# Kernel tuning notes

Measured on AMD Instinct MI355X. Metric: run time of the kernel, lower is better.

Reference implementation:

```python
import jax, jax.numpy as jnp
import numpy as np

N_NODES = 100000


def gcn_layer(x, W, b, src, dst, norm, n):
    # x: [N, Fin] -> linear transform then normalized scatter-add aggregation
    h = x @ W                                   # [N, Fout]
    msgs = h[src] * norm[:, None]               # [E+N, Fout] edge messages
    out = jax.ops.segment_sum(msgs, dst, num_segments=n)
    return out + b


def _build_graph(edge_index, n):
    # add self loops (PyG GCNConv default)
    loops = jnp.arange(n, dtype=edge_index.dtype)
    src = jnp.concatenate([edge_index[0], loops])
    dst = jnp.concatenate([edge_index[1], loops])
    deg = jax.ops.segment_sum(jnp.ones_like(dst, dtype=jnp.float32), dst, num_segments=n)
    dis = jnp.where(deg > 0, jax.lax.rsqrt(deg), 0.0)  # deg^{-1/2}
    norm = dis[src] * dis[dst]                  # symmetric normalization per edge
    return src, dst, norm


def setup_inputs() -> dict:
    key = jax.random.key(0)
    ks = jax.random.split(key, 8)
    x = jax.random.normal(ks[0], (N_NODES, 3), dtype=jnp.float32)
    edge_index = jax.random.randint(ks[1], (2, 6400000), 0, N_NODES, dtype=jnp.int32)
    def glorot(k, fin, fout):
        s = jnp.sqrt(6.0 / (fin + fout))
        return jax.random.uniform(k, (fin, fout), jnp.float32, -s, s)
    return {
        "x": x,
        "edge_index": edge_index,
        "W1": glorot(ks[2], 3, 32), "b1": jnp.zeros((32,), jnp.float32),
        "W2": glorot(ks[3], 32, 32), "b2": jnp.zeros((32,), jnp.float32),
        "W3": glorot(ks[4], 32, 1), "b3": jnp.zeros((1,), jnp.float32),
    }


def reference(x, edge_index, W1, b1, W2, b2, W3, b3):
    n = x.shape[0]
    src, dst, norm = _build_graph(edge_index, n)
    h = jax.nn.relu(gcn_layer(x, W1, b1, src, dst, norm, n))
    h = jax.nn.relu(gcn_layer(h, W2, b2, src, dst, norm, n))
    return gcn_layer(h, W3, b3, src, dst, norm, n)
```

## Files before the change

### kernel.cpp

```cpp
#include <hip/hip_runtime.h>
#include <hip/hip_fp16.h>


#define BLK 256
#define SB 1280
#define CHUNK 5000
#define BKT 128
#define NBKT 782
#define MAXNB 1024
#define BUFSZ 15360

__global__ void k_hist(const int* __restrict__ dst, int* __restrict__ hist, int E) {
    __shared__ int lh[NBKT];
    for (int b = threadIdx.x; b < NBKT; b += blockDim.x) lh[b] = 0;
    __syncthreads();
    int beg = blockIdx.x * CHUNK;
    int end = min(E, beg + CHUNK);
    int nq = (end - beg) >> 2;
    const int4* d4 = (const int4*)(dst + beg);
    for (int i = threadIdx.x; i < nq; i += blockDim.x) {
        int4 d = d4[i];
        atomicAdd(&lh[d.x >> 7], 1);
        atomicAdd(&lh[d.y >> 7], 1);
        atomicAdd(&lh[d.z >> 7], 1);
        atomicAdd(&lh[d.w >> 7], 1);
    }
    for (int e = beg + (nq << 2) + threadIdx.x; e < end; e += blockDim.x)
        atomicAdd(&lh[dst[e] >> 7], 1);
    __syncthreads();
    for (int b = threadIdx.x; b < NBKT; b += blockDim.x)
        hist[(size_t)blockIdx.x * NBKT + b] = lh[b];
}

__global__ void k_scanA(const int* __restrict__ hist, int* __restrict__ histX,
                        int* __restrict__ btot, int NB) {
    int b = blockIdx.x, t = threadIdx.x;
    int base = t * 5;
    int v0 = hist[(size_t)(base + 0) * NB + b];
    int v1 = hist[(size_t)(base + 1) * NB + b];
    int v2 = hist[(size_t)(base + 2) * NB + b];
    int v3 = hist[(size_t)(base + 3) * NB + b];
    int v4 = hist[(size_t)(base + 4) * NB + b];
    int s = v0 + v1 + v2 + v3 + v4;
    int lane = t & 63, w = t >> 6;
    int x = s;
#pragma unroll
    for (int off = 1; off < 64; off <<= 1) {
        int u = __shfl_up(x, off, 64);
        if (lane >= off) x += u;
    }
    __shared__ int wsum[4];
    if (lane == 63) wsum[w] = x;
    __syncthreads();
    int woff = 0;
    for (int k = 0; k < 4; k++) woff += (k < w) ? wsum[k] : 0;
    int run = woff + x - s;
    histX[(size_t)(base + 0) * NB + b] = run;  run += v0;
    histX[(size_t)(base + 1) * NB + b] = run;  run += v1;
    histX[(size_t)(base + 2) * NB + b] = run;  run += v2;
    histX[(size_t)(base + 3) * NB + b] = run;  run += v3;
    histX[(size_t)(base + 4) * NB + b] = run;  run += v4;
    if (t == 255) btot[b] = run;
}

__global__ void k_scanB(const int* __restrict__ btot, int* __restrict__ bbase,
                        int NB, int E) {
    __shared__ int sh[MAXNB];
    int t = threadIdx.x;
    int v = (t < NB) ? btot[t] : 0;
    sh[t] = v;
    __syncthreads();
    for (int off = 1; off < MAXNB; off <<= 1) {
        int u = (t >= off) ? sh[t - off] : 0;
        __syncthreads();
        sh[t] += u;
        __syncthreads();
    }
    if (t < NB) bbase[t] = sh[t] - v;
    if (t == 0) bbase[NB] = E;
}

__global__ void k_bsort(const int* __restrict__ src, const int* __restrict__ dst,
                        const int* __restrict__ hist, const int* __restrict__ histX,
                        const int* __restrict__ bbase,
                        unsigned int* __restrict__ packed, int E) {
    __shared__ unsigned int bufB[CHUNK];
    __shared__ unsigned short binarr2[CHUNK];
    __shared__ int cnt[NBKT];
    __shared__ int off[NBKT];
    __shared__ int cur[NBKT];
    __shared__ int gbase[NBKT];
    __shared__ int wsum[4];
    int t = threadIdx.x;
    int beg = blockIdx.x * CHUNK;
    int end = min(E, beg + CHUNK);
    int len = end - beg;
    for (int b = t; b < NBKT; b += blockDim.x) {
        cnt[b] = hist[(size_t)blockIdx.x * NBKT + b];
        gbase[b] = bbase[b] + histX[(size_t)blockIdx.x * NBKT + b];
    }
    __syncthreads();
    {
        int base = t * 4;
        int v0 = (base + 0 < NBKT) ? cnt[base + 0] : 0;
        int v1 = (base + 1 < NBKT) ? cnt[base + 1] : 0;
        int v2 = (base + 2 < NBKT) ? cnt[base + 2] : 0;
        int v3 = (base + 3 < NBKT) ? cnt[base + 3] : 0;
        int s = v0 + v1 + v2 + v3;
        int lane = t & 63, w = t >> 6;
        int x = s;
#pragma unroll
        for (int o = 1; o < 64; o <<= 1) {
            int u = __shfl_up(x, o, 64);
            if (lane >= o) x += u;
        }
        if (lane == 63) wsum[w] = x;
        __syncthreads();
        int woff = 0;
        for (int k = 0; k < 4; k++) woff += (k < w) ? wsum[k] : 0;
        int run = woff + x - s;
        if (base + 0 < NBKT) { off[base + 0] = run; cur[base + 0] = run; } run += v0;
        if (base + 1 < NBKT) { off[base + 1] = run; cur[base + 1] = run; } run += v1;
        if (base + 2 < NBKT) { off[base + 2] = run; cur[base + 2] = run; } run += v2;
        if (base + 3 < NBKT) { off[base + 3] = run; cur[base + 3] = run; } run += v3;
    }
    __syncthreads();
    for (int i = t; i < len; i += blockDim.x) {
        int d = dst[beg + i];
        int s = src[beg + i];
        int b = d >> 7;
        int pos = atomicAdd(&cur[b], 1);
        bufB[pos] = (unsigned)s | ((unsigned)(d & 127) << 17);
        binarr2[pos] = (unsigned short)b;
    }
    __syncthreads();
    for (int i = t; i < len; i += blockDim.x) {
        int b = binarr2[i];
        packed[gbase[b] + i - off[b]] = bufB[i];
    }
}

__global__ void k_sort(unsigned int* __restrict__ packed, const int* __restrict__ bbase,
                       const float* __restrict__ x, float* __restrict__ dis,
                       float4* __restrict__ y4, int* __restrict__ rowptr, int N, int E) {
    __shared__ unsigned int buf[BUFSZ];
    __shared__ int cnt[BKT];
    __shared__ int sc[BKT];
    __shared__ int cur[BKT];
    int b = blockIdx.x, t = threadIdx.x;
    int beg = bbase[b], end = bbase[b + 1];
    int len = end - beg;
    for (int i = t; i < len; i += blockDim.x) buf[i] = packed[beg + i];
    if (t < BKT) cnt[t] = 0;
    __syncthreads();
    for (int i = t; i < len; i += blockDim.x)
        atomicAdd(&cnt[buf[i] >> 17], 1);
    __syncthreads();
    int v = 0;
    if (t < BKT) { v = cnt[t]; sc[t] = v; }
    __syncthreads();
    for (int off = 1; off < BKT; off <<= 1) {
        int u = 0;
        if (t < BKT && t >= off) u = sc[t - off];
        __syncthreads();
        if (t < BKT) sc[t] += u;
        __syncthreads();
    }
    if (t < BKT) {
        int excl = sc[t] - v;
        cur[t] = excl;
        int gi = b * BKT + t;
        if (gi < N) {
            rowptr[gi] = beg + excl;
            float di = rsqrtf((float)v + 1.0f);
            dis[gi] = di;
            float4 y;
            y.x = di * x[3 * gi + 0];
            y.y = di * x[3 * gi + 1];
            y.z = di * x[3 * gi + 2];
            y.w = 0.0f;
            y4[gi] = y;
        }
    }
    __syncthreads();
    for (int i = t; i < len; i += blockDim.x) {
        unsigned vv = buf[i];
        int pos = atomicAdd(&cur[vv >> 17], 1);
        packed[beg + pos] = vv & 0x1FFFF;
    }
    if (b == 0 && t == 0) rowptr[N] = E;
}

__global__ void k_l1(const unsigned int* __restrict__ csr, const int* __restrict__ rowptr,
                     const float4* __restrict__ y4, const float* __restrict__ dis,
                     const float* __restrict__ W1, const float* __restrict__ b1,
                     __half* __restrict__ g, int N) {
    int t = blockIdx.x * blockDim.x + threadIdx.x;
    int i = t >> 5, j = t & 31;
    if (i >= N) return;
    int beg = rowptr[i], end = rowptr[i + 1];
    float ax = 0.f, ay = 0.f, az = 0.f;
    for (int e = beg + j; e < end; e += 32) {
        float4 yv = y4[__builtin_nontemporal_load(&csr[e])];
        ax += yv.x; ay += yv.y; az += yv.z;
    }
#pragma unroll
    for (int m = 16; m >= 1; m >>= 1) {
        ax += __shfl_xor(ax, m, 32);
        ay += __shfl_xor(ay, m, 32);
        az += __shfl_xor(az, m, 32);
    }
    float di = dis[i];
    float4 ys = y4[i];
    float a0 = di * (ax + ys.x);
    float a1 = di * (ay + ys.y);
    float a2 = di * (az + ys.z);
    float h = b1[j] + a0 * W1[j] + a1 * W1[32 + j] + a2 * W1[64 + j];
    g[(size_t)i * 32 + j] = __float2half(di * fmaxf(h, 0.f));
}

__global__ void k_l2(const unsigned int* __restrict__ csr, const int* __restrict__ rowptr,
                     const __half* __restrict__ g, const float* __restrict__ dis,
                     const float* __restrict__ W2, const float* __restrict__ b2,
                     const float* __restrict__ W3, float* __restrict__ q, int N) {
    int t = blockIdx.x * blockDim.x + threadIdx.x;
    int i = t >> 5, j = t & 31;
    if (i >= N) return;
    int beg = rowptr[i], end = rowptr[i + 1];
    float a0 = 0.f, a1 = 0.f, a2 = 0.f, a3 = 0.f;
    float a4 = 0.f, a5 = 0.f, a6 = 0.f, a7 = 0.f;
    for (int k0 = beg; k0 < end; k0 += 32) {
        int e = k0 + j;
        int myedge = (e < end) ? (int)__builtin_nontemporal_load(&csr[e]) : 0;
        int cnt = min(32, end - k0);
        int t2 = 0;
        for (; t2 + 8 <= cnt; t2 += 8) {
            int s0 = __shfl(myedge, t2 + 0, 32);
            int s1 = __shfl(myedge, t2 + 1, 32);
            int s2 = __shfl(myedge, t2 + 2, 32);
            int s3 = __shfl(myedge, t2 + 3, 32);
            int s4 = __shfl(myedge, t2 + 4, 32);
            int s5 = __shfl(myedge, t2 + 5, 32);
            int s6 = __shfl(myedge, t2 + 6, 32);
            int s7 = __shfl(myedge, t2 + 7, 32);
            a0 += __half2float(g[(size_t)s0 * 32 + j]);
            a1 += __half2float(g[(size_t)s1 * 32 + j]);
            a2 += __half2float(g[(size_t)s2 * 32 + j]);
            a3 += __half2float(g[(size_t)s3 * 32 + j]);
            a4 += __half2float(g[(size_t)s4 * 32 + j]);
            a5 += __half2float(g[(size_t)s5 * 32 + j]);
            a6 += __half2float(g[(size_t)s6 * 32 + j]);
            a7 += __half2float(g[(size_t)s7 * 32 + j]);
        }
        for (; t2 < cnt; t2++) {
            int s = __shfl(myedge, t2, 32);
            a0 += __half2float(g[(size_t)s * 32 + j]);
        }
    }
    float acc = ((a0 + a1) + (a2 + a3)) + ((a4 + a5) + (a6 + a7));
    float di = dis[i];
    float a = di * (acc + __half2float(g[(size_t)i * 32 + j]));
    float o = b2[j];
#pragma unroll
    for (int k = 0; k < 32; k++)
        o += __shfl(a, k, 32) * W2[k * 32 + j];
    float h2 = fmaxf(o, 0.f);
    float c = h2 * W3[j];
#pragma unroll
    for (int m = 16; m >= 1; m >>= 1)
        c += __shfl_xor(c, m, 32);
    if (j == 0) q[i] = di * c;
}

__global__ void k_l3(const unsigned int* __restrict__ csr, const int* __restrict__ rowptr,
                     const float* __restrict__ q, const float* __restrict__ dis,
                     const float* __restrict__ b3, float* __restrict__ out, int N) {
    int t = blockIdx.x * blockDim.x + threadIdx.x;
    int i = t >> 5, j = t & 31;
    if (i >= N) return;
    int beg = rowptr[i], end = rowptr[i + 1];
    float acc = 0.f;
    for (int e = beg + j; e < end; e += 32)
        acc += q[__builtin_nontemporal_load(&csr[e])];
#pragma unroll
    for (int m = 16; m >= 1; m >>= 1)
        acc += __shfl_xor(acc, m, 32);
    if (j == 0) out[i] = dis[i] * (acc + q[i]) + b3[0];
}

extern "C" void kernel_launch(void* const* d_in, const int* in_sizes, int n_in,
                              void* d_out, int out_size, void* d_ws, size_t ws_size,
                              hipStream_t stream) {
    const float* x  = (const float*)d_in[0];
    const int*   ei = (const int*)d_in[1];
    const float* W1 = (const float*)d_in[2];
    const float* b1 = (const float*)d_in[3];
    const float* W2 = (const float*)d_in[4];
    const float* b2 = (const float*)d_in[5];
    const float* W3 = (const float*)d_in[6];
    const float* b3 = (const float*)d_in[7];
    float* out = (float*)d_out;

    int N = in_sizes[0] / 3;
    int E = in_sizes[1] / 2;
    const int* src = ei;
    const int* dst = ei + E;

    char* w = (char*)d_ws;
    int*   hist   = (int*)w;       w += (size_t)SB * NBKT * 4;
    int*   histX  = (int*)w;       w += (size_t)SB * NBKT * 4;
    int*   btot   = (int*)w;       w += (size_t)MAXNB * 4;
    int*   bbase  = (int*)w;       w += (size_t)(MAXNB + 1) * 4;
    int*   rowptr = (int*)w;       w += (size_t)(N + 1) * 4;
    float* dis    = (float*)w;     w += (size_t)N * 4;
    float* y4     = (float*)w;     w += (size_t)N * 16;
    __half* g     = (__half*)w;    w += (size_t)N * 32 * 2;
    float* q      = (float*)w;     w += (size_t)N * 4;
    unsigned int* packed = (unsigned int*)w;  w += (size_t)E * 4;

    k_hist <<<SB, BLK, 0, stream>>>(dst, hist, E);
    k_scanA<<<NBKT, BLK, 0, stream>>>(hist, histX, btot, NBKT);
    k_scanB<<<1, MAXNB, 0, stream>>>(btot, bbase, NBKT, E);
    k_bsort<<<SB, BLK, 0, stream>>>(src, dst, hist, histX, bbase, packed, E);
    k_sort <<<NBKT, BLK, 0, stream>>>(packed, bbase, x, dis, (float4*)y4, rowptr, N, E);

    long long tn32 = (long long)N * 32;
    unsigned gn32 = (unsigned)((tn32 + BLK - 1) / BLK);
    k_l1<<<gn32, BLK, 0, stream>>>(packed, rowptr, (const float4*)y4, dis, W1, b1, g, N);
    k_l2<<<gn32, BLK, 0, stream>>>(packed, rowptr, g, dis, W2, b2, W3, q, N);
    k_l3<<<gn32, BLK, 0, stream>>>(packed, rowptr, q, dis, b3, out, N);
}
```

Baseline: 379.7 us.

## Split bucket sort into count and permute kernels, fusing layer-1 aggregation

```diff
diff --git a/kernel.cpp b/kernel.cpp
--- a/kernel.cpp
+++ b/kernel.cpp
@@ -8,7 +8,7 @@
 #define BKT 128
 #define NBKT 782
 #define MAXNB 1024
-#define BUFSZ 15360
+#define CAP 44
 
 __global__ void k_hist(const int* __restrict__ dst, int* __restrict__ hist, int E) {
     __shared__ int lh[NBKT];
@@ -140,21 +140,17 @@
     }
 }
 
-__global__ void k_sort(unsigned int* __restrict__ packed, const int* __restrict__ bbase,
-                       const float* __restrict__ x, float* __restrict__ dis,
-                       float4* __restrict__ y4, int* __restrict__ rowptr, int N, int E) {
-    __shared__ unsigned int buf[BUFSZ];
+__global__ void k_cnt(const unsigned int* __restrict__ packed, const int* __restrict__ bbase,
+                      const float* __restrict__ x, float* __restrict__ dis,
+                      float4* __restrict__ y4, int* __restrict__ rowptr, int N, int E) {
     __shared__ int cnt[BKT];
     __shared__ int sc[BKT];
-    __shared__ int cur[BKT];
     int b = blockIdx.x, t = threadIdx.x;
     int beg = bbase[b], end = bbase[b + 1];
-    int len = end - beg;
-    for (int i = t; i < len; i += blockDim.x) buf[i] = packed[beg + i];
     if (t < BKT) cnt[t] = 0;
     __syncthreads();
-    for (int i = t; i < len; i += blockDim.x)
-        atomicAdd(&cnt[buf[i] >> 17], 1);
+    for (int i = beg + t; i < end; i += blockDim.x)
+        atomicAdd(&cnt[packed[i] >> 17], 1);
     __syncthreads();
     int v = 0;
     if (t < BKT) { v = cnt[t]; sc[t] = v; }
@@ -167,11 +163,9 @@
         __syncthreads();
     }
     if (t < BKT) {
-        int excl = sc[t] - v;
-        cur[t] = excl;
         int gi = b * BKT + t;
         if (gi < N) {
-            rowptr[gi] = beg + excl;
+            rowptr[gi] = beg + sc[t] - v;
             float di = rsqrtf((float)v + 1.0f);
             dis[gi] = di;
             float4 y;
@@ -182,41 +176,57 @@
             y4[gi] = y;
         }
     }
-    __syncthreads();
-    for (int i = t; i < len; i += blockDim.x) {
-        unsigned vv = buf[i];
-        int pos = atomicAdd(&cur[vv >> 17], 1);
-        packed[beg + pos] = vv & 0x1FFFF;
-    }
     if (b == 0 && t == 0) rowptr[N] = E;
 }
 
-__global__ void k_l1(const unsigned int* __restrict__ csr, const int* __restrict__ rowptr,
-                     const float4* __restrict__ y4, const float* __restrict__ dis,
-                     const float* __restrict__ W1, const float* __restrict__ b1,
-                     __half* __restrict__ g, int N) {
-    int t = blockIdx.x * blockDim.x + threadIdx.x;
-    int i = t >> 5, j = t & 31;
-    if (i >= N) return;
-    int beg = rowptr[i], end = rowptr[i + 1];
-    float ax = 0.f, ay = 0.f, az = 0.f;
-    for (int e = beg + j; e < end; e += 32) {
-        float4 yv = y4[__builtin_nontemporal_load(&csr[e])];
-        ax += yv.x; ay += yv.y; az += yv.z;
-    }
-#pragma unroll
-    for (int m = 16; m >= 1; m >>= 1) {
-        ax += __shfl_xor(ax, m, 32);
-        ay += __shfl_xor(ay, m, 32);
-        az += __shfl_xor(az, m, 32);
-    }
-    float di = dis[i];
-    float4 ys = y4[i];
-    float a0 = di * (ax + ys.x);
-    float a1 = di * (ay + ys.y);
-    float a2 = di * (az + ys.z);
-    float h = b1[j] + a0 * W1[j] + a1 * W1[32 + j] + a2 * W1[64 + j];
-    g[(size_t)i * 32 + j] = __float2half(di * fmaxf(h, 0.f));
+__global__ void k_perm(unsigned int* __restrict__ packed, const int* __restrict__ bbase,
+                       const int* __restrict__ rowptr,
+                       const float4* __restrict__ y4, const float* __restrict__ dis,
+                       const float* __restrict__ W1, const float* __restrict__ b1,
+                       __half* __restrict__ g, int N) {
+    __shared__ int cur[BKT];
+    __shared__ float acc[BKT * 4];
+    int b = blockIdx.x, t = threadIdx.x;
+    int beg = bbase[b], end = bbase[b + 1];
+    int len = end - beg;
+    if (t < BKT) {
+        int gi = b * BKT + t;
+        cur[t] = (gi < N ? rowptr[gi] : beg) - beg;
+    }
+    for (int i = t; i < BKT * 4; i += blockDim.x) acc[i] = 0.f;
+    unsigned ed[CAP];
+#pragma unroll
+    for (int k = 0; k < CAP; k++) {
+        int i = t + k * BLK;
+        ed[k] = (i < len) ? packed[beg + i] : 0xFFFFFFFFu;
+    }
+    __syncthreads();
+#pragma unroll
+    for (int k = 0; k < CAP; k++) {
+        unsigned v = ed[k];
+        if (v != 0xFFFFFFFFu) {
+            int s = v & 0x1FFFF, l = v >> 17;
+            int pos = atomicAdd(&cur[l], 1);
+            packed[beg + pos] = (unsigned)s;
+            float4 y = y4[s];
+            atomicAdd(&acc[l * 4 + 0], y.x);
+            atomicAdd(&acc[l * 4 + 1], y.y);
+            atomicAdd(&acc[l * 4 + 2], y.z);
+        }
+    }
+    __syncthreads();
+    int j = t & 31;
+    for (int n = t >> 5; n < BKT; n += BLK >> 5) {
+        int gi = b * BKT + n;
+        if (gi >= N) break;
+        float di = dis[gi];
+        float4 ys = y4[gi];
+        float a0 = di * (acc[n * 4 + 0] + ys.x);
+        float a1 = di * (acc[n * 4 + 1] + ys.y);
+        float a2 = di * (acc[n * 4 + 2] + ys.z);
+        float h = b1[j] + a0 * W1[j] + a1 * W1[32 + j] + a2 * W1[64 + j];
+        g[(size_t)gi * 32 + j] = __float2half(di * fmaxf(h, 0.f));
+    }
 }
 
 __global__ void k_l2(const unsigned int* __restrict__ csr, const int* __restrict__ rowptr,
@@ -231,7 +241,7 @@
     float a4 = 0.f, a5 = 0.f, a6 = 0.f, a7 = 0.f;
     for (int k0 = beg; k0 < end; k0 += 32) {
         int e = k0 + j;
-        int myedge = (e < end) ? (int)__builtin_nontemporal_load(&csr[e]) : 0;
+        int myedge = (e < end) ? (int)csr[e] : 0;
         int cnt = min(32, end - k0);
         int t2 = 0;
         for (; t2 + 8 <= cnt; t2 += 8) {
@@ -281,7 +291,7 @@
     int beg = rowptr[i], end = rowptr[i + 1];
     float acc = 0.f;
     for (int e = beg + j; e < end; e += 32)
-        acc += q[__builtin_nontemporal_load(&csr[e])];
+        acc += q[csr[e]];
 #pragma unroll
     for (int m = 16; m >= 1; m >>= 1)
         acc += __shfl_xor(acc, m, 32);
@@ -322,11 +332,12 @@
     k_scanA<<<NBKT, BLK, 0, stream>>>(hist, histX, btot, NBKT);
     k_scanB<<<1, MAXNB, 0, stream>>>(btot, bbase, NBKT, E);
     k_bsort<<<SB, BLK, 0, stream>>>(src, dst, hist, histX, bbase, packed, E);
-    k_sort <<<NBKT, BLK, 0, stream>>>(packed, bbase, x, dis, (float4*)y4, rowptr, N, E);
+    k_cnt  <<<NBKT, BLK, 0, stream>>>(packed, bbase, x, dis, (float4*)y4, rowptr, N, E);
+    k_perm <<<NBKT, BLK, 0, stream>>>(packed, bbase, rowptr, (const float4*)y4, dis,
+                                      W1, b1, g, N);
 
     long long tn32 = (long long)N * 32;
     unsigned gn32 = (unsigned)((tn32 + BLK - 1) / BLK);
-    k_l1<<<gn32, BLK, 0, stream>>>(packed, rowptr, (const float4*)y4, dis, W1, b1, g, N);
     k_l2<<<gn32, BLK, 0, stream>>>(packed, rowptr, g, dis, W2, b2, W3, q, N);
     k_l3<<<gn32, BLK, 0, stream>>>(packed, rowptr, q, dis, b3, out, N);
 }
```

New measurement: 432.5 us. 1.14x slower.
